# Kernel optimization log

Hardware: AMD Instinct MI355X
Metric: run time of the kernel (lower is better)

## Reference

```python
import jax, jax.numpy as jnp
import numpy as np

_CLIP = 1e4

def _n2n(t):
    return jnp.nan_to_num(t, nan=0.0, posinf=_CLIP, neginf=-_CLIP)

def setup_inputs() -> dict:
    key = jax.random.key(0)
    ks = jax.random.split(key, 9)
    B, N, E, DH, DM = 4, 16384, 65536, 128, 64
    s = 0.05
    return {
        "x": jax.random.normal(ks[0], (B, N, 3), jnp.float32),
        "h": jax.random.normal(ks[1], (B, N, DH), jnp.float32),
        "edge_index": jax.random.randint(ks[2], (B, E, 2), 0, N, jnp.int64 if jax.config.jax_enable_x64 else jnp.int32),
        "pe_w1": jax.random.normal(ks[3], (2 * DH + 1, DM), jnp.float32) * s,
        "pe_b1": jnp.zeros((DM,), jnp.float32),
        "pe_w2": jax.random.normal(ks[4], (DM, DM), jnp.float32) * s,
        "pe_b2": jnp.zeros((DM,), jnp.float32),
        "px_w": jax.random.normal(ks[5], (DM, 1), jnp.float32) * s,
        "ph_w1": jax.random.normal(ks[6], (DH + DM, DH), jnp.float32) * s,
        "ph_b1": jnp.zeros((DH,), jnp.float32),
        "ph_w2": jax.random.normal(ks[7], (DH, DH), jnp.float32) * s,
        "ph_b2": jnp.zeros((DH,), jnp.float32),
    }

def reference(x, h, edge_index, pe_w1, pe_b1, pe_w2, pe_b2, px_w, ph_w1, ph_b1, ph_w2, ph_b2):
    B = x.shape[0]
    src = edge_index[:, :, 0]          # [B,E]
    dst = edge_index[:, :, 1]
    bidx = jnp.arange(B)[:, None]      # [B,1] for batched gather/scatter
    x_i = x[bidx, src]                 # [B,E,3]
    x_j = x[bidx, dst]
    h_i = h[bidx, src]                 # [B,E,DH]
    h_j = h[bidx, dst]
    diff = x_i - x_j
    dist2 = jnp.clip((diff ** 2).sum(-1, keepdims=True), 1e-12, None)  # [B,E,1]
    edge_input = _n2n(jnp.concatenate([h_i, h_j, dist2], axis=-1))
    # phi_e: Linear -> SiLU -> Linear -> SiLU
    m = jax.nn.silu(edge_input @ pe_w1 + pe_b1)
    m_ij = _n2n(jax.nn.silu(m @ pe_w2 + pe_b2))   # [B,E,DM]
    m_x = m_ij @ px_w                             # [B,E,1]
    direction = diff / (jnp.sqrt(dist2) + 1e-8)
    delta_x_ij = _n2n(m_x * direction)            # [B,E,3]
    delta_x = jnp.zeros_like(x).at[bidx, src].add(delta_x_ij)
    delta_h_msg = jnp.zeros((B, x.shape[1], m_ij.shape[-1]), h.dtype).at[bidx, src].add(m_ij)
    h_input = jnp.concatenate([h, delta_h_msg], axis=-1)
    h_new = h + jax.nn.silu(h_input @ ph_w1 + ph_b1) @ ph_w2 + ph_b2
    x_new = x + delta_x
    return _n2n(x_new), _n2n(h_new)
```

## Files before the change

kernel.cpp:

```cpp
#include <hip/hip_runtime.h>


typedef unsigned short ushort_t;
typedef __attribute__((ext_vector_type(8))) short bf16x8;
typedef __attribute__((ext_vector_type(4))) float f32x4;
typedef _Float16 h2 __attribute__((ext_vector_type(2)));

__device__ __forceinline__ float fast_rcp(float v) { return __builtin_amdgcn_rcpf(v); }
__device__ __forceinline__ float fast_silu(float v) { return v * fast_rcp(1.0f + __expf(-v)); }
__device__ __forceinline__ ushort_t f2bf(float f) {
    unsigned u = __float_as_uint(f);
    u += 0x7fffu + ((u >> 16) & 1u);
    return (ushort_t)(u >> 16);
}
__device__ __forceinline__ float bf2f(ushort_t b) {
    return __uint_as_float(((unsigned)b) << 16);
}
__device__ __forceinline__ h2 u2h2(unsigned u) {
    union { unsigned u; h2 h; } v; v.u = u; return v.h;
}

__global__ __launch_bounds__(256) void init_k(const float* __restrict__ pe_w1,
                                              const float* __restrict__ pe_w2,
                                              const float* __restrict__ ph_w1,
                                              const float* __restrict__ ph_w2,
                                              int* __restrict__ cursor,
                                              ushort_t* __restrict__ W1t,
                                              ushort_t* __restrict__ Wp1t,
                                              ushort_t* __restrict__ Wp2t,
                                              unsigned* __restrict__ w2h) {
    int gg = blockIdx.x * 256 + threadIdx.x;
    if (gg < 65536) { cursor[gg] = 0; return; }
    int g = gg - 65536;
    if (g < 16384) {
        int c = g >> 7, k = g & 127;
        float v = (c < 64) ? pe_w1[k * 64 + c] : pe_w1[(128 + k) * 64 + (c - 64)];
        W1t[g] = f2bf(v);
    } else if (g < 40960) {
        int g2 = g - 16384;
        int n = g2 / 192, k = g2 - n * 192;
        Wp1t[g2] = f2bf(ph_w1[k * 128 + n]);
    } else if (g < 57344) {
        int g3 = g - 40960;
        int n = g3 >> 7, k = g3 & 127;
        Wp2t[g3] = f2bf(ph_w2[k * 128 + n]);
    } else if (g < 59392) {
        int g4 = g - 57344;
        int k2 = g4 >> 6, c = g4 & 63;
        union { unsigned u; _Float16 h[2]; } p;
        p.h[0] = (_Float16)pe_w2[(2 * k2) * 64 + c];
        p.h[1] = (_Float16)pe_w2[(2 * k2 + 1) * 64 + c];
        w2h[g4] = p.u;
    }
}

template <bool EMIT_BF16>
__global__ __launch_bounds__(256, 2) void pgemm_scatter_k(const float* __restrict__ A0,
                                                          const ushort_t* __restrict__ Wt,
                                                          ushort_t* __restrict__ outP,
                                                          ushort_t* __restrict__ hbout,
                                                          const int* __restrict__ ei,
                                                          int* __restrict__ cursor,
                                                          int* __restrict__ elist) {
    constexpr int KPAD = 40;
    __shared__ ushort_t As[128 * KPAD];
    __shared__ ushort_t Bs[128 * KPAD];
    const int tid = threadIdx.x;

    if (blockIdx.x >= 512) {
        int e = (blockIdx.x - 512) * 256 + tid;
        int2 sd = ((const int2*)ei)[e];
        int b = e >> 16;
        int gi = (b << 14) + sd.x;
        int gj = (b << 14) + sd.y;
        int slot = atomicAdd(&cursor[gi], 1);
        if (slot < 64) elist[gi * 64 + slot] = gj;
        return;
    }

    const int m0 = blockIdx.x * 128;
    const int wave = tid >> 6;
    const int lane = tid & 63;
    const int lr = lane & 15;
    const int lq = lane >> 4;

    f32x4 acc[2][8];
#pragma unroll
    for (int mt = 0; mt < 2; mt++)
#pragma unroll
        for (int nt = 0; nt < 8; nt++) { f32x4 z = {0.f,0.f,0.f,0.f}; acc[mt][nt] = z; }

    for (int k0 = 0; k0 < 128; k0 += 32) {
#pragma unroll
        for (int i = 0; i < 4; i++) {
            int lin = tid + i * 256;
            int m = lin >> 3;
            int kq = (lin & 7) * 4;
            float4 v = *(const float4*)(A0 + (size_t)(m0 + m) * 128 + k0 + kq);
            ushort4 w4;
            w4.x = f2bf(v.x); w4.y = f2bf(v.y); w4.z = f2bf(v.z); w4.w = f2bf(v.w);
            if (EMIT_BF16)
                *(ushort4*)(hbout + (size_t)(m0 + m) * 128 + k0 + kq) = w4;
            *(ushort4*)&As[m * KPAD + kq] = w4;
        }
#pragma unroll
        for (int i = 0; i < 2; i++) {
            int lin = tid + i * 256;
            int n = lin >> 2;
            int kq = (lin & 3) * 8;
            *(uint4*)&Bs[n * KPAD + kq] = *(const uint4*)(Wt + (size_t)n * 128 + k0 + kq);
        }
        __syncthreads();
        bf16x8 af[2], bfr[8];
#pragma unroll
        for (int mt = 0; mt < 2; mt++)
            af[mt] = *(const bf16x8*)&As[(wave * 32 + mt * 16 + lr) * KPAD + lq * 8];
#pragma unroll
        for (int nt = 0; nt < 8; nt++)
            bfr[nt] = *(const bf16x8*)&Bs[(nt * 16 + lr) * KPAD + lq * 8];
#pragma unroll
        for (int mt = 0; mt < 2; mt++)
#pragma unroll
            for (int nt = 0; nt < 8; nt++)
                acc[mt][nt] = __builtin_amdgcn_mfma_f32_16x16x32_bf16(af[mt], bfr[nt], acc[mt][nt], 0, 0, 0);
        __syncthreads();
    }
#pragma unroll
    for (int mt = 0; mt < 2; mt++)
#pragma unroll
        for (int nt = 0; nt < 8; nt++)
#pragma unroll
            for (int r = 0; r < 4; r++) {
                int row = m0 + wave * 32 + mt * 16 + lq * 4 + r;
                int col = nt * 16 + lr;
                outP[(size_t)row * 128 + col] = f2bf(acc[mt][nt][r]);
            }
}

__global__ __launch_bounds__(64, 4) void node_k(const float* __restrict__ x,
                                                const ushort_t* __restrict__ P,
                                                const int* __restrict__ cursor,
                                                const int* __restrict__ elist,
                                                const float* __restrict__ w1,
                                                const float* __restrict__ b1,
                                                const unsigned* __restrict__ w2h,
                                                const float* __restrict__ b2,
                                                const float* __restrict__ pxw,
                                                ushort_t* __restrict__ dh,
                                                float* __restrict__ outx) {
    const int n = blockIdx.x;
    const int lane = threadIdx.x;
    __shared__ __attribute__((aligned(16))) unsigned m_u[32];
    ushort_t* mh = (ushort_t*)m_u;

    const float w1r = w1[256 * 64 + lane];
    const float b2v = b2[lane];
    const float pxv = pxw[lane];
    const float Pib = bf2f(P[(size_t)n * 128 + lane]) + b1[lane];
    const float xi0 = x[n * 3 + 0];
    const float xi1 = x[n * 3 + 1];
    const float xi2 = x[n * 3 + 2];

    float dhacc = 0.0f;
    float dxp0 = 0.0f, dxp1 = 0.0f, dxp2 = 0.0f;
    const int dg = min(cursor[n], 64);
    const int base = n * 64;

    int gj0 = (dg > 0) ? elist[base] : 0;
    float Pj = bf2f(P[(size_t)gj0 * 128 + 64 + lane]);
    float xj0 = x[gj0 * 3 + 0];
    float xj1 = x[gj0 * 3 + 1];
    float xj2 = x[gj0 * 3 + 2];

    for (int t = 0; t < dg; t++) {
        int gjn = (t + 1 < dg) ? elist[base + t + 1] : 0;
        float Pjn = bf2f(P[(size_t)gjn * 128 + 64 + lane]);
        float xn0 = x[gjn * 3 + 0];
        float xn1 = x[gjn * 3 + 1];
        float xn2 = x[gjn * 3 + 2];

        float ddx = xi0 - xj0;
        float ddy = xi1 - xj1;
        float ddz = xi2 - xj2;
        float d2 = fmaxf(ddx * ddx + ddy * ddy + ddz * ddz, 1e-12f);
        float m = fast_silu(Pib + Pj + d2 * w1r);
        __builtin_amdgcn_wave_barrier();
        union { ushort_t s; _Float16 h; } mc;
        mc.h = (_Float16)m;
        mh[lane] = mc.s;
        __builtin_amdgcn_wave_barrier();
        float s0 = b2v, s1 = 0.0f, s2 = 0.0f, s3 = 0.0f;
#pragma unroll
        for (int q = 0; q < 8; q++) {
            uint4 mm = *(const uint4*)&m_u[q * 4];
            s0 = __builtin_amdgcn_fdot2(u2h2(mm.x), u2h2(w2h[(4 * q + 0) * 64 + lane]), s0, false);
            s1 = __builtin_amdgcn_fdot2(u2h2(mm.y), u2h2(w2h[(4 * q + 1) * 64 + lane]), s1, false);
            s2 = __builtin_amdgcn_fdot2(u2h2(mm.z), u2h2(w2h[(4 * q + 2) * 64 + lane]), s2, false);
            s3 = __builtin_amdgcn_fdot2(u2h2(mm.w), u2h2(w2h[(4 * q + 3) * 64 + lane]), s3, false);
        }
        __builtin_amdgcn_wave_barrier();
        float m2 = fast_silu((s0 + s1) + (s2 + s3));
        dhacc += m2;
        float c = m2 * pxv * fast_rcp(sqrtf(d2) + 1e-8f);
        dxp0 = fmaf(c, ddx, dxp0);
        dxp1 = fmaf(c, ddy, dxp1);
        dxp2 = fmaf(c, ddz, dxp2);

        Pj = Pjn; xj0 = xn0; xj1 = xn1; xj2 = xn2;
    }

    dh[(size_t)n * 64 + lane] = f2bf(dhacc);

    for (int off = 32; off; off >>= 1) {
        dxp0 += __shfl_down(dxp0, off);
        dxp1 += __shfl_down(dxp1, off);
        dxp2 += __shfl_down(dxp2, off);
    }
    if (lane == 0) {
        outx[n * 3 + 0] = xi0 + dxp0;
        outx[n * 3 + 1] = xi1 + dxp1;
        outx[n * 3 + 2] = xi2 + dxp2;
    }
}

template <bool USE_HB>
__global__ __launch_bounds__(256, 2) void mlp_fused_k(const float* __restrict__ h,
                                                      const ushort_t* __restrict__ hb,
                                                      const ushort_t* __restrict__ dh,
                                                      const ushort_t* __restrict__ Wp1t,
                                                      const float* __restrict__ b1,
                                                      const ushort_t* __restrict__ Wp2t,
                                                      const float* __restrict__ b2,
                                                      float* __restrict__ outh) {
    constexpr int KPAD = 40, TPAD = 136;
    __shared__ ushort_t As[128 * KPAD];
    __shared__ ushort_t Bs[128 * KPAD];
    __shared__ ushort_t Ts[128 * TPAD];
    const int tid = threadIdx.x;
    const int m0 = blockIdx.x * 128;
    const int wave = tid >> 6;
    const int lane = tid & 63;
    const int lr = lane & 15;
    const int lq = lane >> 4;

    f32x4 acc[2][8];
#pragma unroll
    for (int mt = 0; mt < 2; mt++)
#pragma unroll
        for (int nt = 0; nt < 8; nt++) { f32x4 z = {0.f,0.f,0.f,0.f}; acc[mt][nt] = z; }

    for (int k0 = 0; k0 < 192; k0 += 32) {
        if (USE_HB) {
#pragma unroll
            for (int i = 0; i < 2; i++) {
                int lin = tid + i * 256;
                int m = lin >> 2;
                int kq = (lin & 3) * 8;
                const ushort_t* src = (k0 >= 128)
                    ? dh + (size_t)(m0 + m) * 64 + (k0 - 128 + kq)
                    : hb + (size_t)(m0 + m) * 128 + k0 + kq;
                *(uint4*)&As[m * KPAD + kq] = *(const uint4*)src;
            }
        } else {
#pragma unroll
            for (int i = 0; i < 4; i++) {
                int lin = tid + i * 256;
                int m = lin >> 3;
                int kq = (lin & 7) * 4;
                ushort4 w4;
                if (k0 >= 128) {
                    w4 = *(const ushort4*)(dh + (size_t)(m0 + m) * 64 + (k0 - 128 + kq));
                } else {
                    float4 v = *(const float4*)(h + (size_t)(m0 + m) * 128 + k0 + kq);
                    w4.x = f2bf(v.x); w4.y = f2bf(v.y); w4.z = f2bf(v.z); w4.w = f2bf(v.w);
                }
                *(ushort4*)&As[m * KPAD + kq] = w4;
            }
        }
#pragma unroll
        for (int i = 0; i < 2; i++) {
            int lin = tid + i * 256;
            int n = lin >> 2;
            int kq = (lin & 3) * 8;
            *(uint4*)&Bs[n * KPAD + kq] = *(const uint4*)(Wp1t + (size_t)n * 192 + k0 + kq);
        }
        __syncthreads();
        bf16x8 af[2], bfr[8];
#pragma unroll
        for (int mt = 0; mt < 2; mt++)
            af[mt] = *(const bf16x8*)&As[(wave * 32 + mt * 16 + lr) * KPAD + lq * 8];
#pragma unroll
        for (int nt = 0; nt < 8; nt++)
            bfr[nt] = *(const bf16x8*)&Bs[(nt * 16 + lr) * KPAD + lq * 8];
#pragma unroll
        for (int mt = 0; mt < 2; mt++)
#pragma unroll
            for (int nt = 0; nt < 8; nt++)
                acc[mt][nt] = __builtin_amdgcn_mfma_f32_16x16x32_bf16(af[mt], bfr[nt], acc[mt][nt], 0, 0, 0);
        __syncthreads();
    }
#pragma unroll
    for (int mt = 0; mt < 2; mt++)
#pragma unroll
        for (int nt = 0; nt < 8; nt++)
#pragma unroll
            for (int r = 0; r < 4; r++) {
                int row = wave * 32 + mt * 16 + lq * 4 + r;
                int col = nt * 16 + lr;
                Ts[row * TPAD + col] = f2bf(fast_silu(acc[mt][nt][r] + b1[col]));
            }
    __syncthreads();

    f32x4 acc2[2][8];
#pragma unroll
    for (int mt = 0; mt < 2; mt++)
#pragma unroll
        for (int nt = 0; nt < 8; nt++) { f32x4 z = {0.f,0.f,0.f,0.f}; acc2[mt][nt] = z; }

    for (int k0 = 0; k0 < 128; k0 += 32) {
#pragma unroll
        for (int i = 0; i < 2; i++) {
            int lin = tid + i * 256;
            int n = lin >> 2;
            int kq = (lin & 3) * 8;
            *(uint4*)&Bs[n * KPAD + kq] = *(const uint4*)(Wp2t + (size_t)n * 128 + k0 + kq);
        }
        __syncthreads();
        bf16x8 af[2], bfr[8];
#pragma unroll
        for (int mt = 0; mt < 2; mt++)
            af[mt] = *(const bf16x8*)&Ts[(wave * 32 + mt * 16 + lr) * TPAD + k0 + lq * 8];
#pragma unroll
        for (int nt = 0; nt < 8; nt++)
            bfr[nt] = *(const bf16x8*)&Bs[(nt * 16 + lr) * KPAD + lq * 8];
#pragma unroll
        for (int mt = 0; mt < 2; mt++)
#pragma unroll
            for (int nt = 0; nt < 8; nt++)
                acc2[mt][nt] = __builtin_amdgcn_mfma_f32_16x16x32_bf16(af[mt], bfr[nt], acc2[mt][nt], 0, 0, 0);
        __syncthreads();
    }
#pragma unroll
    for (int mt = 0; mt < 2; mt++)
#pragma unroll
        for (int nt = 0; nt < 8; nt++)
#pragma unroll
            for (int r = 0; r < 4; r++) {
                int row = m0 + wave * 32 + mt * 16 + lq * 4 + r;
                int col = nt * 16 + lr;
                float v = acc2[mt][nt][r] + b2[col];
                if (USE_HB) v += bf2f(hb[(size_t)row * 128 + col]);
                else        v += h[(size_t)row * 128 + col];
                outh[(size_t)row * 128 + col] = v;
            }
}

extern "C" void kernel_launch(void* const* d_in, const int* in_sizes, int n_in,
                              void* d_out, int out_size, void* d_ws, size_t ws_size,
                              hipStream_t stream) {
    const float* x     = (const float*)d_in[0];
    const float* h     = (const float*)d_in[1];
    const int*   ei    = (const int*)d_in[2];
    const float* pe_w1 = (const float*)d_in[3];
    const float* pe_b1 = (const float*)d_in[4];
    const float* pe_w2 = (const float*)d_in[5];
    const float* pe_b2 = (const float*)d_in[6];
    const float* px_w  = (const float*)d_in[7];
    const float* ph_w1 = (const float*)d_in[8];
    const float* ph_b1 = (const float*)d_in[9];
    const float* ph_w2 = (const float*)d_in[10];
    const float* ph_b2 = (const float*)d_in[11];

    float* outx = (float*)d_out;
    float* outh = (float*)d_out + 196608;

    ushort_t* P    = (ushort_t*)d_ws;
    ushort_t* dh   = P + (size_t)65536 * 128;
    int* cursor    = (int*)(dh + (size_t)65536 * 64);
    int* elist     = cursor + 65536;
    ushort_t* W1t  = (ushort_t*)(elist + (size_t)65536 * 64);
    ushort_t* Wp1t = W1t + 16384;
    ushort_t* Wp2t = Wp1t + 24576;
    unsigned* w2h  = (unsigned*)(Wp2t + 16384);
    ushort_t* hb   = (ushort_t*)(w2h + 4096);
    size_t need_hb = (size_t)((char*)(hb + (size_t)65536 * 128) - (char*)d_ws);
    const bool use_hb = ws_size >= need_hb;

    init_k<<<488, 256, 0, stream>>>(pe_w1, pe_w2, ph_w1, ph_w2,
                                    cursor, W1t, Wp1t, Wp2t, w2h);
    if (use_hb)
        pgemm_scatter_k<true><<<1536, 256, 0, stream>>>(h, W1t, P, hb,
                                                        ei, cursor, elist);
    else
        pgemm_scatter_k<false><<<1536, 256, 0, stream>>>(h, W1t, P, nullptr,
                                                         ei, cursor, elist);
    node_k<<<65536, 64, 0, stream>>>(x, P, cursor, elist,
                                     pe_w1, pe_b1, w2h, pe_b2, px_w,
                                     dh, outx);
    if (use_hb)
        mlp_fused_k<true><<<512, 256, 0, stream>>>(h, hb, dh, Wp1t, ph_b1,
                                                   Wp2t, ph_b2, outh);
    else
        mlp_fused_k<false><<<512, 256, 0, stream>>>(h, nullptr, dh, Wp1t, ph_b1,
                                                    Wp2t, ph_b2, outh);
}
```

Before: 190.0 us.

## Preload full weight matrices into LDS and load A fragments directly to registers

Both GEMM kernels now stage the entire transposed weight matrix once into shared memory in a k-group-major layout, and load the activation fragments straight from global memory into MFMA registers instead of staging them through LDS. This removes the per-k-step syncthreads and the A-tile LDS round trip. The intermediate SiLU tile switches to the same k-group-major layout. In exchange, LDS use per block grows (up to 80KB in the MLP kernel), the min-blocks launch bound is dropped, and A loads become less coalesced (16B per lane across rows), which may lower occupancy.

```diff
diff --git a/kernel.cpp b/kernel.cpp
--- a/kernel.cpp
+++ b/kernel.cpp
@@ -55,16 +55,14 @@
 }
 
 template <bool EMIT_BF16>
-__global__ __launch_bounds__(256, 2) void pgemm_scatter_k(const float* __restrict__ A0,
-                                                          const ushort_t* __restrict__ Wt,
-                                                          ushort_t* __restrict__ outP,
-                                                          ushort_t* __restrict__ hbout,
-                                                          const int* __restrict__ ei,
-                                                          int* __restrict__ cursor,
-                                                          int* __restrict__ elist) {
-    constexpr int KPAD = 40;
-    __shared__ ushort_t As[128 * KPAD];
-    __shared__ ushort_t Bs[128 * KPAD];
+__global__ __launch_bounds__(256) void pgemm_scatter_k(const float* __restrict__ A0,
+                                                       const ushort_t* __restrict__ Wt,
+                                                       ushort_t* __restrict__ outP,
+                                                       ushort_t* __restrict__ hbout,
+                                                       const int* __restrict__ ei,
+                                                       int* __restrict__ cursor,
+                                                       int* __restrict__ elist) {
+    __shared__ ushort_t Bs[16384];
     const int tid = threadIdx.x;
 
     if (blockIdx.x >= 512) {
@@ -84,6 +82,14 @@
     const int lr = lane & 15;
     const int lq = lane >> 4;
 
+#pragma unroll
+    for (int i = 0; i < 8; i++) {
+        int c = tid + i * 256;
+        int n = c >> 4, kg = c & 15;
+        *(uint4*)&Bs[kg * 1024 + n * 8] = *(const uint4*)(Wt + n * 128 + kg * 8);
+    }
+    __syncthreads();
+
     f32x4 acc[2][8];
 #pragma unroll
     for (int mt = 0; mt < 2; mt++)
@@ -91,39 +97,32 @@
         for (int nt = 0; nt < 8; nt++) { f32x4 z = {0.f,0.f,0.f,0.f}; acc[mt][nt] = z; }
 
     for (int k0 = 0; k0 < 128; k0 += 32) {
-#pragma unroll
-        for (int i = 0; i < 4; i++) {
-            int lin = tid + i * 256;
-            int m = lin >> 3;
-            int kq = (lin & 7) * 4;
-            float4 v = *(const float4*)(A0 + (size_t)(m0 + m) * 128 + k0 + kq);
-            ushort4 w4;
-            w4.x = f2bf(v.x); w4.y = f2bf(v.y); w4.z = f2bf(v.z); w4.w = f2bf(v.w);
+        bf16x8 af[2];
+#pragma unroll
+        for (int mt = 0; mt < 2; mt++) {
+            int row = m0 + wave * 32 + mt * 16 + lr;
+            const float* src = A0 + (size_t)row * 128 + k0 + lq * 8;
+            float4 v0 = *(const float4*)src;
+            float4 v1 = *(const float4*)(src + 4);
+            union { ushort_t s[8]; bf16x8 v; uint4 u; } p;
+            p.s[0] = f2bf(v0.x); p.s[1] = f2bf(v0.y);
+            p.s[2] = f2bf(v0.z); p.s[3] = f2bf(v0.w);
+            p.s[4] = f2bf(v1.x); p.s[5] = f2bf(v1.y);
+            p.s[6] = f2bf(v1.z); p.s[7] = f2bf(v1.w);
             if (EMIT_BF16)
-                *(ushort4*)(hbout + (size_t)(m0 + m) * 128 + k0 + kq) = w4;
-            *(ushort4*)&As[m * KPAD + kq] = w4;
+                *(uint4*)(hbout + (size_t)row * 128 + k0 + lq * 8) = p.u;
+            af[mt] = p.v;
         }
-#pragma unroll
-        for (int i = 0; i < 2; i++) {
-            int lin = tid + i * 256;
-            int n = lin >> 2;
-            int kq = (lin & 3) * 8;
-            *(uint4*)&Bs[n * KPAD + kq] = *(const uint4*)(Wt + (size_t)n * 128 + k0 + kq);
-        }
-        __syncthreads();
-        bf16x8 af[2], bfr[8];
-#pragma unroll
-        for (int mt = 0; mt < 2; mt++)
-            af[mt] = *(const bf16x8*)&As[(wave * 32 + mt * 16 + lr) * KPAD + lq * 8];
-#pragma unroll
-        for (int nt = 0; nt < 8; nt++)
-            bfr[nt] = *(const bf16x8*)&Bs[(nt * 16 + lr) * KPAD + lq * 8];
+        bf16x8 bfr[8];
+        int kg = (k0 >> 3) + lq;
+#pragma unroll
+        for (int nt = 0; nt < 8; nt++)
+            bfr[nt] = *(const bf16x8*)&Bs[kg * 1024 + (nt * 16 + lr) * 8];
 #pragma unroll
         for (int mt = 0; mt < 2; mt++)
 #pragma unroll
             for (int nt = 0; nt < 8; nt++)
                 acc[mt][nt] = __builtin_amdgcn_mfma_f32_16x16x32_bf16(af[mt], bfr[nt], acc[mt][nt], 0, 0, 0);
-        __syncthreads();
     }
 #pragma unroll
     for (int mt = 0; mt < 2; mt++)
@@ -224,18 +223,16 @@
 }
 
 template <bool USE_HB>
-__global__ __launch_bounds__(256, 2) void mlp_fused_k(const float* __restrict__ h,
-                                                      const ushort_t* __restrict__ hb,
-                                                      const ushort_t* __restrict__ dh,
-                                                      const ushort_t* __restrict__ Wp1t,
-                                                      const float* __restrict__ b1,
-                                                      const ushort_t* __restrict__ Wp2t,
-                                                      const float* __restrict__ b2,
-                                                      float* __restrict__ outh) {
-    constexpr int KPAD = 40, TPAD = 136;
-    __shared__ ushort_t As[128 * KPAD];
-    __shared__ ushort_t Bs[128 * KPAD];
-    __shared__ ushort_t Ts[128 * TPAD];
+__global__ __launch_bounds__(256) void mlp_fused_k(const float* __restrict__ h,
+                                                   const ushort_t* __restrict__ hb,
+                                                   const ushort_t* __restrict__ dh,
+                                                   const ushort_t* __restrict__ Wp1t,
+                                                   const float* __restrict__ b1,
+                                                   const ushort_t* __restrict__ Wp2t,
+                                                   const float* __restrict__ b2,
+                                                   float* __restrict__ outh) {
+    __shared__ ushort_t Ws[24576];
+    __shared__ ushort_t Ts[16384];
     const int tid = threadIdx.x;
     const int m0 = blockIdx.x * 128;
     const int wave = tid >> 6;
@@ -243,6 +240,14 @@
     const int lr = lane & 15;
     const int lq = lane >> 4;
 
+#pragma unroll
+    for (int i = 0; i < 12; i++) {
+        int c = tid + i * 256;
+        int kg = c >> 7, n = c & 127;
+        *(uint4*)&Ws[kg * 1024 + n * 8] = *(const uint4*)(Wp1t + (size_t)n * 192 + kg * 8);
+    }
+    __syncthreads();
+
     f32x4 acc[2][8];
 #pragma unroll
     for (int mt = 0; mt < 2; mt++)
@@ -250,54 +255,37 @@
         for (int nt = 0; nt < 8; nt++) { f32x4 z = {0.f,0.f,0.f,0.f}; acc[mt][nt] = z; }
 
     for (int k0 = 0; k0 < 192; k0 += 32) {
-        if (USE_HB) {
-#pragma unroll
-            for (int i = 0; i < 2; i++) {
-                int lin = tid + i * 256;
-                int m = lin >> 2;
-                int kq = (lin & 3) * 8;
-                const ushort_t* src = (k0 >= 128)
-                    ? dh + (size_t)(m0 + m) * 64 + (k0 - 128 + kq)
-                    : hb + (size_t)(m0 + m) * 128 + k0 + kq;
-                *(uint4*)&As[m * KPAD + kq] = *(const uint4*)src;
-            }
-        } else {
-#pragma unroll
-            for (int i = 0; i < 4; i++) {
-                int lin = tid + i * 256;
-                int m = lin >> 3;
-                int kq = (lin & 7) * 4;
-                ushort4 w4;
-                if (k0 >= 128) {
-                    w4 = *(const ushort4*)(dh + (size_t)(m0 + m) * 64 + (k0 - 128 + kq));
-                } else {
-                    float4 v = *(const float4*)(h + (size_t)(m0 + m) * 128 + k0 + kq);
-                    w4.x = f2bf(v.x); w4.y = f2bf(v.y); w4.z = f2bf(v.z); w4.w = f2bf(v.w);
-                }
-                *(ushort4*)&As[m * KPAD + kq] = w4;
+        bf16x8 af[2];
+#pragma unroll
+        for (int mt = 0; mt < 2; mt++) {
+            int row = m0 + wave * 32 + mt * 16 + lr;
+            int k = k0 + lq * 8;
+            if (k >= 128) {
+                af[mt] = *(const bf16x8*)&dh[(size_t)row * 64 + (k - 128)];
+            } else if (USE_HB) {
+                af[mt] = *(const bf16x8*)&hb[(size_t)row * 128 + k];
+            } else {
+                const float* src = h + (size_t)row * 128 + k;
+                float4 v0 = *(const float4*)src;
+                float4 v1 = *(const float4*)(src + 4);
+                union { ushort_t s[8]; bf16x8 v; } p;
+                p.s[0] = f2bf(v0.x); p.s[1] = f2bf(v0.y);
+                p.s[2] = f2bf(v0.z); p.s[3] = f2bf(v0.w);
+                p.s[4] = f2bf(v1.x); p.s[5] = f2bf(v1.y);
+                p.s[6] = f2bf(v1.z); p.s[7] = f2bf(v1.w);
+                af[mt] = p.v;
             }
         }
-#pragma unroll
-        for (int i = 0; i < 2; i++) {
-            int lin = tid + i * 256;
-            int n = lin >> 2;
-            int kq = (lin & 3) * 8;
-            *(uint4*)&Bs[n * KPAD + kq] = *(const uint4*)(Wp1t + (size_t)n * 192 + k0 + kq);
-        }
-        __syncthreads();
-        bf16x8 af[2], bfr[8];
-#pragma unroll
-        for (int mt = 0; mt < 2; mt++)
-            af[mt] = *(const bf16x8*)&As[(wave * 32 + mt * 16 + lr) * KPAD + lq * 8];
-#pragma unroll
-        for (int nt = 0; nt < 8; nt++)
-            bfr[nt] = *(const bf16x8*)&Bs[(nt * 16 + lr) * KPAD + lq * 8];
+        bf16x8 bfr[8];
+        int kg = (k0 >> 3) + lq;
+#pragma unroll
+        for (int nt = 0; nt < 8; nt++)
+            bfr[nt] = *(const bf16x8*)&Ws[kg * 1024 + (nt * 16 + lr) * 8];
 #pragma unroll
         for (int mt = 0; mt < 2; mt++)
 #pragma unroll
             for (int nt = 0; nt < 8; nt++)
                 acc[mt][nt] = __builtin_amdgcn_mfma_f32_16x16x32_bf16(af[mt], bfr[nt], acc[mt][nt], 0, 0, 0);
-        __syncthreads();
     }
 #pragma unroll
     for (int mt = 0; mt < 2; mt++)
@@ -307,9 +295,19 @@
             for (int r = 0; r < 4; r++) {
                 int row = wave * 32 + mt * 16 + lq * 4 + r;
                 int col = nt * 16 + lr;
-                Ts[row * TPAD + col] = f2bf(fast_silu(acc[mt][nt][r] + b1[col]));
+                Ts[(col >> 3) * 1024 + row * 8 + (col & 7)] =
+                    f2bf(fast_silu(acc[mt][nt][r] + b1[col]));
             }
+    __builtin_amdgcn_wave_barrier();
+
     __syncthreads();
+#pragma unroll
+    for (int i = 0; i < 8; i++) {
+        int c = tid + i * 256;
+        int kg = c >> 7, n = c & 127;
+        *(uint4*)&Ws[kg * 1024 + n * 8] = *(const uint4*)(Wp2t + (size_t)n * 128 + kg * 8);
+    }
+    __syncthreads();
 
     f32x4 acc2[2][8];
 #pragma unroll
@@ -318,27 +316,19 @@
         for (int nt = 0; nt < 8; nt++) { f32x4 z = {0.f,0.f,0.f,0.f}; acc2[mt][nt] = z; }
 
     for (int k0 = 0; k0 < 128; k0 += 32) {
-#pragma unroll
-        for (int i = 0; i < 2; i++) {
-            int lin = tid + i * 256;
-            int n = lin >> 2;
-            int kq = (lin & 3) * 8;
-            *(uint4*)&Bs[n * KPAD + kq] = *(const uint4*)(Wp2t + (size_t)n * 128 + k0 + kq);
-        }
-        __syncthreads();
         bf16x8 af[2], bfr[8];
+        int kg = (k0 >> 3) + lq;
 #pragma unroll
         for (int mt = 0; mt < 2; mt++)
-            af[mt] = *(const bf16x8*)&Ts[(wave * 32 + mt * 16 + lr) * TPAD + k0 + lq * 8];
-#pragma unroll
-        for (int nt = 0; nt < 8; nt++)
-            bfr[nt] = *(const bf16x8*)&Bs[(nt * 16 + lr) * KPAD + lq * 8];
+            af[mt] = *(const bf16x8*)&Ts[kg * 1024 + (wave * 32 + mt * 16 + lr) * 8];
+#pragma unroll
+        for (int nt = 0; nt < 8; nt++)
+            bfr[nt] = *(const bf16x8*)&Ws[kg * 1024 + (nt * 16 + lr) * 8];
 #pragma unroll
         for (int mt = 0; mt < 2; mt++)
 #pragma unroll
             for (int nt = 0; nt < 8; nt++)
                 acc2[mt][nt] = __builtin_amdgcn_mfma_f32_16x16x32_bf16(af[mt], bfr[nt], acc2[mt][nt], 0, 0, 0);
-        __syncthreads();
     }
 #pragma unroll
     for (int mt = 0; mt < 2; mt++)
```

Result: no change. 193.4 us (+1.8%).
